# Performance work log

Measured on AMD Instinct MI355X. Metric: run time of the kernel, lower is better.

The kernel has to match this reference:

```python
import jax, jax.numpy as jnp
import numpy as np

N_NODES = 10000
N_EDGES = 100000
F_NODE = 128
F_EDGE = 16
HEADS = 8
OUT_CH = 128  # per-head channels in PyG TransformerConv
HC = HEADS * OUT_CH


def setup_inputs() -> dict:
    key = jax.random.key(0)
    ks = jax.random.split(key, 12)
    sN = 1.0 / np.sqrt(F_NODE)
    sE = 1.0 / np.sqrt(F_EDGE)
    return {
        "x": jax.random.normal(ks[0], (N_NODES, F_NODE), dtype=jnp.float32),
        "edge_attr": jax.random.normal(ks[1], (N_EDGES, F_EDGE), dtype=jnp.float32),
        "edge_index": jax.random.randint(ks[2], (2, N_EDGES), 0, N_NODES, dtype=jnp.int32),
        "Wq": jax.random.normal(ks[3], (F_NODE, HC), dtype=jnp.float32) * sN,
        "bq": jnp.zeros((HC,), dtype=jnp.float32),
        "Wk": jax.random.normal(ks[4], (F_NODE, HC), dtype=jnp.float32) * sN,
        "bk": jnp.zeros((HC,), dtype=jnp.float32),
        "Wv": jax.random.normal(ks[5], (F_NODE, HC), dtype=jnp.float32) * sN,
        "bv": jnp.zeros((HC,), dtype=jnp.float32),
        "We": jax.random.normal(ks[6], (F_EDGE, HC), dtype=jnp.float32) * sE,  # lin_edge has no bias in PyG
        "Wskip": jax.random.normal(ks[7], (F_NODE, OUT_CH), dtype=jnp.float32) * sN,
        "bskip": jnp.zeros((OUT_CH,), dtype=jnp.float32),
        "Wd": jax.random.normal(ks[8], (OUT_CH, 1), dtype=jnp.float32) * (1.0 / np.sqrt(OUT_CH)),
        "bd": jnp.zeros((1,), dtype=jnp.float32),
    }


def reference(x, edge_attr, edge_index, Wq, bq, Wk, bk, Wv, bv, We, Wskip, bskip, Wd, bd):
    N = x.shape[0]
    src, dst = edge_index[0], edge_index[1]  # messages flow src -> dst

    q = (x @ Wq + bq).reshape(N, HEADS, OUT_CH)
    k = (x @ Wk + bk).reshape(N, HEADS, OUT_CH)
    v = (x @ Wv + bv).reshape(N, HEADS, OUT_CH)
    e = (edge_attr @ We).reshape(-1, HEADS, OUT_CH)  # [E, H, C]

    k_j = k[src] + e                        # [E, H, C]
    alpha = jnp.einsum("ehc,ehc->eh", q[dst], k_j) / np.sqrt(OUT_CH)  # [E, H]

    # segment softmax over destination node
    m = jax.ops.segment_max(alpha, dst, num_segments=N)   # [N, H]
    a = jnp.exp(alpha - m[dst])
    s = jax.ops.segment_sum(a, dst, num_segments=N)       # [N, H]
    alpha_n = a / (s[dst] + 1e-16)                        # [E, H]

    msg = (v[src] + e) * alpha_n[:, :, None]              # [E, H, C]
    out = jax.ops.segment_sum(msg, dst, num_segments=N)   # [N, H, C]

    out = out.mean(axis=1)                                # concat=False -> head average, [N, C]
    out = out + x @ Wskip + bskip                         # root/skip connection
    out = jax.nn.relu(out)
    # dropout is identity at inference
    pooled = out.sum(axis=0)                              # [C]
    return pooled @ Wd + bd                               # [1]
```

## Files before the change

### kernel.cpp

```cpp
#include <hip/hip_runtime.h>

#define N_NODES 10000
#define N_EDGES 100000
#define F_NODE 128
#define HEADS 8
#define HC 1024
#define NCOLS2 2432
#define NB2 (NCOLS2 / 128)
#define SLOT_CAP 48

typedef __attribute__((ext_vector_type(8))) short bf16x8;
typedef __attribute__((ext_vector_type(4))) float f32x4;
typedef __attribute__((ext_vector_type(2))) float f32x2;

__device__ __forceinline__ void atomAddF(float* p, float v) {
    unsafeAtomicAdd(p, v);
}
__device__ __forceinline__ unsigned short f2bf(float f) {
    union { float f; unsigned u; } c; c.f = f;
    unsigned u = c.u + 0x7fffu + ((c.u >> 16) & 1u);
    return (unsigned short)(u >> 16);
}
__device__ __forceinline__ float bLo(unsigned x) {
    union { unsigned u; float f; } c; c.u = x << 16; return c.f;
}
__device__ __forceinline__ float bHi(unsigned x) {
    union { unsigned u; float f; } c; c.u = x & 0xffff0000u; return c.f;
}
__device__ __forceinline__ float bf2f(unsigned short u) {
    union { unsigned u; float f; } c; c.u = ((unsigned)u) << 16; return c.f;
}
__device__ __forceinline__ unsigned pk4fp8(unsigned a, unsigned b) {
    int w = __builtin_amdgcn_cvt_pk_fp8_f32(bLo(a), bHi(a), 0, false);
    w = __builtin_amdgcn_cvt_pk_fp8_f32(bLo(b), bHi(b), w, true);
    return (unsigned)w;
}
__device__ __forceinline__ void dq16v(uint4 q, f32x2* f) {
    f[0] = __builtin_amdgcn_cvt_pk_f32_fp8(q.x, false);
    f[1] = __builtin_amdgcn_cvt_pk_f32_fp8(q.x, true);
    f[2] = __builtin_amdgcn_cvt_pk_f32_fp8(q.y, false);
    f[3] = __builtin_amdgcn_cvt_pk_f32_fp8(q.y, true);
    f[4] = __builtin_amdgcn_cvt_pk_f32_fp8(q.z, false);
    f[5] = __builtin_amdgcn_cvt_pk_f32_fp8(q.z, true);
    f[6] = __builtin_amdgcn_cvt_pk_f32_fp8(q.w, false);
    f[7] = __builtin_amdgcn_cvt_pk_f32_fp8(q.w, true);
}
__device__ __forceinline__ void edge_accum2(
    uint4 xq4, uint4 vq4, float2 eav, float svv, bool valid,
    const f32x2* gf2, float qwx, float qwy, float du_r, float scale,
    float& s_reg, float& t0, float& t1, f32x2* va2) {
    f32x2 dac;
    dac.x = eav.x * qwx;
    dac.y = eav.y * qwy;
    f32x2 p;
    p = __builtin_amdgcn_cvt_pk_f32_fp8(xq4.x, false); dac += gf2[0] * p;
    p = __builtin_amdgcn_cvt_pk_f32_fp8(xq4.x, true);  dac += gf2[1] * p;
    p = __builtin_amdgcn_cvt_pk_f32_fp8(xq4.y, false); dac += gf2[2] * p;
    p = __builtin_amdgcn_cvt_pk_f32_fp8(xq4.y, true);  dac += gf2[3] * p;
    p = __builtin_amdgcn_cvt_pk_f32_fp8(xq4.z, false); dac += gf2[4] * p;
    p = __builtin_amdgcn_cvt_pk_f32_fp8(xq4.z, true);  dac += gf2[5] * p;
    p = __builtin_amdgcn_cvt_pk_f32_fp8(xq4.w, false); dac += gf2[6] * p;
    p = __builtin_amdgcn_cvt_pk_f32_fp8(xq4.w, true);  dac += gf2[7] * p;
    float d = dac.x + dac.y;
    d += __shfl_xor(d, 1); d += __shfl_xor(d, 2); d += __shfl_xor(d, 4);
    float a = __expf((d + du_r + svv) * scale);
    a = valid ? a : 0.f;
    s_reg += a;
    t0 += a * eav.x; t1 += a * eav.y;
    f32x2 av; av.x = a; av.y = a;
    p = __builtin_amdgcn_cvt_pk_f32_fp8(vq4.x, false); va2[0] += av * p;
    p = __builtin_amdgcn_cvt_pk_f32_fp8(vq4.x, true);  va2[1] += av * p;
    p = __builtin_amdgcn_cvt_pk_f32_fp8(vq4.y, false); va2[2] += av * p;
    p = __builtin_amdgcn_cvt_pk_f32_fp8(vq4.y, true);  va2[3] += av * p;
    p = __builtin_amdgcn_cvt_pk_f32_fp8(vq4.z, false); va2[4] += av * p;
    p = __builtin_amdgcn_cvt_pk_f32_fp8(vq4.z, true);  va2[5] += av * p;
    p = __builtin_amdgcn_cvt_pk_f32_fp8(vq4.w, false); va2[6] += av * p;
    p = __builtin_amdgcn_cvt_pk_f32_fp8(vq4.w, true);  va2[7] += av * p;
}

#define PREP_A 1250
#define PREP_B (PREP_A + NCOLS2 / 2)
#define PREP_C (PREP_B + 10)
#define PREP_D (PREP_C + 64)
__global__ __launch_bounds__(256) void prep_all(
    const float* __restrict__ x, unsigned short* __restrict__ xb,
    unsigned* __restrict__ xf8, const int* __restrict__ ei,
    int* __restrict__ cnt, int2* __restrict__ slots,
    const float* __restrict__ Wq, const float* __restrict__ Wk,
    const float* __restrict__ Wv, const float* __restrict__ Wskip,
    const float* __restrict__ We, const float* __restrict__ bq,
    const float* __restrict__ bk, const float* __restrict__ bv,
    const float* __restrict__ bskip, unsigned short* __restrict__ wt,
    float* __restrict__ bias, unsigned short* __restrict__ w2t) {
    __shared__ float wesh[2][128];
    __shared__ float wqsh[64][129];
    int tid = threadIdx.x;
    if (blockIdx.x < PREP_A) {
        int i = blockIdx.x * 256 + tid;
        float4 f = ((const float4*)x)[i];
        ushort4 o;
        o.x = f2bf(f.x); o.y = f2bf(f.y); o.z = f2bf(f.z); o.w = f2bf(f.w);
        ((ushort4*)xb)[i] = o;
        int w = __builtin_amdgcn_cvt_pk_fp8_f32(f.x, f.y, 0, false);
        w = __builtin_amdgcn_cvt_pk_fp8_f32(f.z, f.w, w, true);
        xf8[i] = (unsigned)w;
        if (i < N_EDGES) {
            int src = ei[i];
            int dst = ei[N_EDGES + i];
            int pos = atomicAdd(&cnt[dst], 1);
            if (pos < SLOT_CAP) slots[(size_t)dst * SLOT_CAP + pos] = make_int2(src, i);
        }
    } else if (blockIdx.x < PREP_B) {
        int bi = blockIdx.x - PREP_A;
        int cid = tid >> 7, d = tid & 127;
        int n = 2 * bi + cid;
        bool panel = (n < 1024) || (n >= 2176 && n < 2304);
        if (panel) {
            int h = (n < 1024) ? (n >> 7) : ((n - 2176) >> 4);
            if (n < 1024) {
                int f2 = n & 127;
                wesh[cid][d] = Wk[(size_t)f2 * HC + h * 128 + d];
            } else {
                int f = (n - 2176) & 15;
                wesh[cid][d] = We[(size_t)f * HC + h * 128 + d];
            }
            float s = 0.f;
            int c_t = tid & 63, r_t = tid >> 6;
            #pragma unroll 2
            for (int half = 0; half < 2; ++half) {
                #pragma unroll
                for (int rr = 0; rr < 32; ++rr) {
                    int r = rr * 4 + r_t;
                    wqsh[c_t][r] = Wq[(size_t)r * HC + h * 128 + half * 64 + c_t];
                }
                __syncthreads();
                #pragma unroll 16
                for (int cc = 0; cc < 64; ++cc)
                    s += wqsh[cc][d] * wesh[cid][half * 64 + cc];
                __syncthreads();
            }
            wt[(size_t)n * 128 + d] = f2bf(s);
        } else {
            float val;
            if (n < 2048) {
                val = Wv[(size_t)d * HC + (n - 1024)];
            } else if (n < 2176) {
                val = Wskip[(size_t)d * 128 + (n - 2048)];
            } else if (n < 2312) {
                int h = n - 2304;
                wesh[cid][d] = bk[h * 128 + d];
                __syncthreads();
                const float* wq = Wq + (size_t)d * HC + h * 128;
                float s = 0.f;
                #pragma unroll
                for (int c = 0; c < 128; ++c) s += wq[c] * wesh[cid][c];
                val = s;
            } else if (n < 2320) {
                int h = n - 2312;
                wesh[cid][d] = bq[h * 128 + d];
                __syncthreads();
                const float* wk = Wk + (size_t)d * HC + h * 128;
                float s = 0.f;
                #pragma unroll
                for (int c = 0; c < 128; ++c) s += wk[c] * wesh[cid][c];
                val = s;
            } else {
                val = 0.f;
            }
            wt[(size_t)n * 128 + d] = f2bf(val);
        }
    } else if (blockIdx.x < PREP_C) {
        int n = (blockIdx.x - PREP_B) * 256 + tid;
        if (n >= NCOLS2) return;
        float val;
        if (n < 1024) val = 0.f;
        else if (n < 2048) val = bv[n - 1024];
        else if (n < 2176) val = bskip[n - 2048];
        else if (n < 2304) {
            int hf = n - 2176, h = hf >> 4, f = hf & 15;
            float s = 0.f;
            for (int c = 0; c < 128; ++c)
                s += bq[h * 128 + c] * We[(size_t)f * HC + h * 128 + c];
            val = s;
        } else if (n < 2312) {
            int h = n - 2304;
            float s = 0.f;
            for (int c = 0; c < 128; ++c) s += bq[h * 128 + c] * bk[h * 128 + c];
            val = s;
        } else val = 0.f;
        bias[n] = val;
    } else {
        int c = (blockIdx.x - PREP_C) * 2 + (tid >> 7);
        int d = tid & 127;
        int h = d >> 4, f = d & 15;
        w2t[(size_t)c * 128 + d] = f2bf(We[(size_t)f * HC + h * 128 + c] * 0.125f);
    }
}

__global__ __launch_bounds__(256) void gemm_mfma(
    const unsigned short* __restrict__ xb, const unsigned short* __restrict__ wt,
    const float* __restrict__ bias, unsigned char* __restrict__ xgf8,
    unsigned char* __restrict__ vf8, unsigned short* __restrict__ sqb,
    float* __restrict__ du, float* __restrict__ sv) {
    __shared__ unsigned short lds[18432];
    unsigned short (*As)[72] = (unsigned short(*)[72])lds;
    unsigned short (*Bs)[72] = (unsigned short(*)[72])(lds + 9216);
    int tid = threadIdx.x;
    int n0 = blockIdx.x * 128, m0 = blockIdx.y * 128;
    int w = tid >> 6, lane = tid & 63;
    int wm = (w >> 1) * 64, wn = (w & 1) * 64;
    int quad = lane >> 4, l16 = lane & 15;
    f32x4 acc[4][4];
    #pragma unroll
    for (int i = 0; i < 4; ++i)
        #pragma unroll
        for (int j = 0; j < 4; ++j) acc[i][j] = (f32x4){0.f, 0.f, 0.f, 0.f};

    for (int ko = 0; ko < 128; ko += 64) {
        #pragma unroll
        for (int tI = 0; tI < 4; ++tI) {
            int cId = tid + tI * 256;
            int r = cId >> 3, c8 = (cId & 7) << 3;
            int gr = m0 + r;
            uint4 av = make_uint4(0u, 0u, 0u, 0u);
            if (gr < N_NODES)
                av = *(const uint4*)(xb + (size_t)gr * 128 + ko + c8);
            *(uint4*)(&As[r][c8]) = av;
            *(uint4*)(&Bs[r][c8]) =
                *(const uint4*)(wt + (size_t)(n0 + r) * 128 + ko + c8);
        }
        __syncthreads();
        #pragma unroll
        for (int ks = 0; ks < 64; ks += 32) {
            bf16x8 a[4], b[4];
            #pragma unroll
            for (int mt = 0; mt < 4; ++mt)
                a[mt] = *(const bf16x8*)&As[wm + mt * 16 + l16][ks + quad * 8];
            #pragma unroll
            for (int nt = 0; nt < 4; ++nt)
                b[nt] = *(const bf16x8*)&Bs[wn + nt * 16 + l16][ks + quad * 8];
            #pragma unroll
            for (int mt = 0; mt < 4; ++mt)
                #pragma unroll
                for (int nt = 0; nt < 4; ++nt)
                    acc[mt][nt] = __builtin_amdgcn_mfma_f32_16x16x32_bf16(
                        a[mt], b[nt], acc[mt][nt], 0, 0, 0);
        }
        __syncthreads();
    }
    int nt0 = n0 >> 7;
    if (nt0 == 18) {
        #pragma unroll
        for (int mt = 0; mt < 4; ++mt)
            #pragma unroll
            for (int r = 0; r < 4; ++r) {
                int row = m0 + wm + mt * 16 + quad * 4 + r;
                if (row >= N_NODES) continue;
                #pragma unroll
                for (int nt = 0; nt < 4; ++nt) {
                    int col = n0 + wn + nt * 16 + l16;
                    float val = acc[mt][nt][r] + bias[col];
                    if (col < 2312) {
                        du[(size_t)row * 8 + (col - 2304)] = val;
                    } else if (col < 2320) {
                        sv[(size_t)row * 8 + (col - 2312)] = val;
                    }
                }
            }
    } else {
        unsigned short* wst = lds + w * 4608;
        #pragma unroll
        for (int mt = 0; mt < 4; ++mt)
            #pragma unroll
            for (int r = 0; r < 4; ++r) {
                int rl = mt * 16 + quad * 4 + r;
                #pragma unroll
                for (int nt = 0; nt < 4; ++nt) {
                    int cl = nt * 16 + l16;
                    wst[rl * 72 + cl] = f2bf(acc[mt][nt][r] + bias[n0 + wn + cl]);
                }
            }
        __syncthreads();
        if (nt0 < 16) {
            unsigned char* dst = (nt0 < 8) ? xgf8 : vf8;
            int colbase = (n0 & 1023);
            #pragma unroll
            for (int j = 0; j < 4; ++j) {
                int idx = tid + j * 256;
                int r = idx >> 3, c16 = idx & 7;
                int wown = ((r >> 6) << 1) | (c16 >> 2);
                int rl = r & 63;
                const unsigned short* srcp =
                    lds + wown * 4608 + rl * 72 + (c16 & 3) * 16;
                uint4 u0 = *(const uint4*)(srcp);
                uint4 u1 = *(const uint4*)(srcp + 8);
                uint4 o;
                o.x = pk4fp8(u0.x, u0.y);
                o.y = pk4fp8(u0.z, u0.w);
                o.z = pk4fp8(u1.x, u1.y);
                o.w = pk4fp8(u1.z, u1.w);
                int row = m0 + r;
                if (row < N_NODES)
                    *(uint4*)(dst + (size_t)row * 1024 + colbase + c16 * 16) = o;
            }
        } else {
            int colbase = n0 - 2048;
            #pragma unroll
            for (int j = 0; j < 4; ++j) {
                int idx = tid + j * 256;
                int r = idx >> 3, c16 = idx & 7;
                int wown = ((r >> 6) << 1) | (c16 >> 2);
                int rl = r & 63;
                const unsigned short* srcp =
                    lds + wown * 4608 + rl * 72 + (c16 & 3) * 16;
                uint4 u0 = *(const uint4*)(srcp);
                uint4 u1 = *(const uint4*)(srcp + 8);
                int row = m0 + r;
                if (row < N_NODES) {
                    uint4* dp = (uint4*)(sqb + (size_t)row * 256 + colbase + c16 * 16);
                    dp[0] = u0;
                    dp[1] = u1;
                }
            }
        }
    }
}

__global__ __launch_bounds__(256) void node_kernel(
    const unsigned char* __restrict__ xgf8, const unsigned char* __restrict__ xf8,
    const unsigned char* __restrict__ vf8, const unsigned short* __restrict__ sqb,
    const float* __restrict__ ea, const float* __restrict__ du,
    const float* __restrict__ sv, const int2* __restrict__ slots,
    const int* __restrict__ cnt, unsigned short* __restrict__ ttb,
    float* __restrict__ hsum) {
    int t = threadIdx.x;
    int w = t >> 6, lane = t & 63;
    int lh = lane & 7, h = lane >> 3;
    const float scale = 0.08838834764831845f;
    int n = __builtin_amdgcn_readfirstlane(blockIdx.x * 4 + w);

    uint4 gq = *(const uint4*)(xgf8 + (size_t)n * 1024 + 16 * lane);
    f32x2 gf2[8];
    dq16v(gq, gf2);
    ushort2 qwu = *(const ushort2*)(sqb + (size_t)n * 256 + 128 + h * 16 + 2 * lh);
    float qwx = bf2f(qwu.x), qwy = bf2f(qwu.y);
    float du_r = du[(size_t)n * 8 + h];

    int cn = cnt[n];
    cn = (cn > SLOT_CAP) ? SLOT_CAP : cn;
    cn = __builtin_amdgcn_readfirstlane(cn);
    const int2* sp = slots + (size_t)n * SLOT_CAP;
    const unsigned char* eab = (const unsigned char*)ea;

    unsigned xoff = lh * 16u;
    unsigned voff = lane * 16u;
    unsigned eoff = lh * 8u;

    f32x2 va2[8];
    #pragma unroll
    for (int i = 0; i < 8; ++i) va2[i] = (f32x2){0.f, 0.f};
    float s_reg = 0.f, t0 = 0.f, t1 = 0.f;

    if (cn > 0) {
        int np = (cn + 1) >> 1;
        uint4 x0A = {}, x0B = {}, v0A = {}, v0B = {};
        uint4 x1A = {}, x1B = {}, v1A = {}, v1B = {};
        float2 e0A = {}, e0B = {}, e1A = {}, e1B = {};
        float sv0A = 0.f, sv0B = 0.f, sv1A = 0.f, sv1B = 0.f;
        bool m0B = false, m1B = false;

#define LOADP(xA, xB, vA, vB, eA, eB, svA, svB, mB, pp) do {                    \
        int _p = (pp);                                                          \
        if (_p < np) {                                                          \
            int _i0 = 2 * _p;                                                   \
            bool _mb = (_i0 + 1) < cn;                                          \
            int2 _sa = sp[_i0];                                                 \
            int2 _sb = sp[_mb ? _i0 + 1 : _i0];                                 \
            mB = _mb;                                                           \
            xA = *(const uint4*)(xf8 + (((unsigned)_sa.x) << 7) + xoff);        \
            xB = *(const uint4*)(xf8 + (((unsigned)_sb.x) << 7) + xoff);        \
            vA = *(const uint4*)(vf8 + (((unsigned)_sa.x) << 10) + voff);       \
            vB = *(const uint4*)(vf8 + (((unsigned)_sb.x) << 10) + voff);       \
            eA = *(const float2*)(eab + (((unsigned)_sa.y) << 6) + eoff);       \
            eB = *(const float2*)(eab + (((unsigned)_sb.y) << 6) + eoff);       \
            svA = sv[(((unsigned)_sa.x) << 3) + h];                             \
            svB = sv[(((unsigned)_sb.x) << 3) + h];                             \
        }                                                                       \
    } while (0)

        LOADP(x0A, x0B, v0A, v0B, e0A, e0B, sv0A, sv0B, m0B, 0);
        LOADP(x1A, x1B, v1A, v1B, e1A, e1B, sv1A, sv1B, m1B, 1);
        int p = 0;
        while (true) {
            if (p >= np) break;
            edge_accum2(x0A, v0A, e0A, sv0A, true, gf2, qwx, qwy, du_r, scale,
                        s_reg, t0, t1, va2);
            edge_accum2(x0B, v0B, e0B, sv0B, m0B, gf2, qwx, qwy, du_r, scale,
                        s_reg, t0, t1, va2);
            LOADP(x0A, x0B, v0A, v0B, e0A, e0B, sv0A, sv0B, m0B, p + 2);
            ++p;
            if (p >= np) break;
            edge_accum2(x1A, v1A, e1A, sv1A, true, gf2, qwx, qwy, du_r, scale,
                        s_reg, t0, t1, va2);
            edge_accum2(x1B, v1B, e1B, sv1B, m1B, gf2, qwx, qwy, du_r, scale,
                        s_reg, t0, t1, va2);
            LOADP(x1A, x1B, v1A, v1B, e1A, e1B, sv1A, sv1B, m1B, p + 2);
            ++p;
        }
#undef LOADP
    }

    float inv = 1.f / (s_reg + 1e-16f);
    ushort2 tw;
    tw.x = f2bf(t0 * inv);
    tw.y = f2bf(t1 * inv);
    *(ushort2*)(ttb + (size_t)n * 128 + h * 16 + 2 * lh) = tw;
    float sc = inv * 0.125f;
    float va[16];
    #pragma unroll
    for (int i = 0; i < 8; ++i) { va[2 * i] = va2[i].x; va[2 * i + 1] = va2[i].y; }
    #pragma unroll
    for (int i = 0; i < 16; ++i) {
        float o = va[i] * sc;
        o += __shfl_xor(o, 8);
        o += __shfl_xor(o, 16);
        o += __shfl_xor(o, 32);
        va[i] = o;
    }
    if (lane < 8) {
        float* hp = hsum + (size_t)n * 128 + lane * 16;
        #pragma unroll
        for (int p2 = 0; p2 < 4; ++p2) {
            float4 h4 = make_float4(va[4 * p2], va[4 * p2 + 1],
                                    va[4 * p2 + 2], va[4 * p2 + 3]);
            ((float4*)hp)[p2] = h4;
        }
    }
}

__global__ __launch_bounds__(256) void out_gemm(
    const unsigned short* __restrict__ ttb, const unsigned short* __restrict__ w2t,
    const float* __restrict__ hsum, const unsigned short* __restrict__ sqb,
    float* __restrict__ pooled, int* __restrict__ done,
    const float* __restrict__ Wd, const float* __restrict__ bd,
    float* __restrict__ out) {
    __shared__ unsigned short As[64][136];
    __shared__ float pool_sh[128];
    __shared__ int last_sh;
    int tid = threadIdx.x;
    int m0 = blockIdx.x * 64;
    int w = tid >> 6, lane = tid & 63;
    int wm = (w >> 1) * 32, wn = (w & 1) * 64;
    int quad = lane >> 4, l16 = lane & 15;
    if (tid < 128) pool_sh[tid] = 0.f;
    #pragma unroll
    for (int tI = 0; tI < 4; ++tI) {
        int cId = tid + tI * 256;
        int r = cId >> 4, c8 = (cId & 15) << 3;
        int gr = m0 + r;
        uint4 av = make_uint4(0u, 0u, 0u, 0u);
        if (gr < N_NODES)
            av = *(const uint4*)(ttb + (size_t)gr * 128 + c8);
        *(uint4*)(&As[r][c8]) = av;
    }
    __syncthreads();
    f32x4 acc[2][4];
    #pragma unroll
    for (int i = 0; i < 2; ++i)
        #pragma unroll
        for (int j = 0; j < 4; ++j) acc[i][j] = (f32x4){0.f, 0.f, 0.f, 0.f};

    const unsigned short* bb = w2t + (size_t)(wn + l16) * 128 + quad * 8;
    #pragma unroll
    for (int ks = 0; ks < 128; ks += 32) {
        bf16x8 a[2], b[4];
        #pragma unroll
        for (int mt = 0; mt < 2; ++mt)
            a[mt] = *(const bf16x8*)&As[wm + mt * 16 + l16][ks + quad * 8];
        #pragma unroll
        for (int nt = 0; nt < 4; ++nt)
            b[nt] = *(const bf16x8*)(bb + (size_t)nt * 16 * 128 + ks);
        #pragma unroll
        for (int mt = 0; mt < 2; ++mt)
            #pragma unroll
            for (int nt = 0; nt < 4; ++nt)
                acc[mt][nt] = __builtin_amdgcn_mfma_f32_16x16x32_bf16(
                    a[mt], b[nt], acc[mt][nt], 0, 0, 0);
    }
    float pl[4] = {0.f, 0.f, 0.f, 0.f};
    #pragma unroll
    for (int mt = 0; mt < 2; ++mt) {
        #pragma unroll
        for (int r = 0; r < 4; ++r) {
            int row = m0 + wm + mt * 16 + quad * 4 + r;
            if (row >= N_NODES) continue;
            #pragma unroll
            for (int nt = 0; nt < 4; ++nt) {
                int col = wn + nt * 16 + l16;
                float val = acc[mt][nt][r] + hsum[(size_t)row * 128 + col]
                            + bf2f(sqb[(size_t)row * 256 + col]);
                pl[nt] += fmaxf(val, 0.f);
            }
        }
    }
    #pragma unroll
    for (int nt = 0; nt < 4; ++nt)
        atomicAdd(&pool_sh[wn + nt * 16 + l16], pl[nt]);
    __syncthreads();
    if (tid < 128) atomAddF(&pooled[tid], pool_sh[tid]);
    __threadfence();
    if (tid == 0) last_sh = (atomicAdd(done, 1) == (int)gridDim.x - 1);
    __syncthreads();
    if (last_sh && tid < 64) {
        float p0 = __hip_atomic_load(&pooled[2 * tid], __ATOMIC_RELAXED,
                                     __HIP_MEMORY_SCOPE_AGENT);
        float p1 = __hip_atomic_load(&pooled[2 * tid + 1], __ATOMIC_RELAXED,
                                     __HIP_MEMORY_SCOPE_AGENT);
        float vv = p0 * Wd[2 * tid] + p1 * Wd[2 * tid + 1];
        vv += __shfl_xor(vv, 1);  vv += __shfl_xor(vv, 2);  vv += __shfl_xor(vv, 4);
        vv += __shfl_xor(vv, 8);  vv += __shfl_xor(vv, 16); vv += __shfl_xor(vv, 32);
        if (tid == 0) out[0] = vv + bd[0];
    }
}

extern "C" void kernel_launch(void* const* d_in, const int* in_sizes, int n_in,
                              void* d_out, int out_size, void* d_ws, size_t ws_size,
                              hipStream_t stream) {
    const float* x     = (const float*)d_in[0];
    const float* eattr = (const float*)d_in[1];
    const int*   ei    = (const int*)d_in[2];
    const float* Wq    = (const float*)d_in[3];
    const float* bq    = (const float*)d_in[4];
    const float* Wk    = (const float*)d_in[5];
    const float* bk    = (const float*)d_in[6];
    const float* Wv    = (const float*)d_in[7];
    const float* bv    = (const float*)d_in[8];
    const float* We    = (const float*)d_in[9];
    const float* Wskip = (const float*)d_in[10];
    const float* bskip = (const float*)d_in[11];
    const float* Wd    = (const float*)d_in[12];
    const float* bd    = (const float*)d_in[13];
    float* out = (float*)d_out;

    char* ws = (char*)d_ws;
    unsigned char*  xgf8 = (unsigned char*)(ws + 0);
    unsigned char*  vf8  = (unsigned char*)(ws + 10240000);
    unsigned short* sqb  = (unsigned short*)(ws + 20480000);
    float* hsum = (float*)(ws + 25600000);
    unsigned short* xb   = (unsigned short*)(ws + 30720000);
    unsigned short* ttb  = xb;
    unsigned*       xf8  = (unsigned*)(ws + 33280000);
    float* du   = (float*)(ws + 34560000);
    float* sv   = (float*)(ws + 34880000);
    unsigned short* wt   = (unsigned short*)(ws + 35200000);
    float* bias = (float*)(ws + 35822592);
    unsigned short* w2t  = (unsigned short*)(ws + 35832320);
    int* cnt    = (int*)(ws + 35865088);
    float* pooled = (float*)(ws + 35905088);
    int* done   = (int*)(ws + 35905600);
    int2* slots = (int2*)(ws + 35905616);

    hipMemsetAsync(cnt, 0, 40000 + 512 + 16, stream);

    prep_all<<<PREP_D, 256, 0, stream>>>(
        x, xb, xf8, ei, cnt, slots, Wq, Wk, Wv, Wskip, We, bq, bk, bv, bskip,
        wt, bias, w2t);

    gemm_mfma<<<dim3(NB2, (N_NODES + 127) / 128), 256, 0, stream>>>(
        xb, wt, bias, xgf8, vf8, sqb, du, sv);

    node_kernel<<<N_NODES / 4, 256, 0, stream>>>(
        xgf8, (const unsigned char*)xf8, vf8, sqb, eattr, du, sv, slots, cnt,
        ttb, hsum);

    out_gemm<<<(N_NODES + 63) / 64, 256, 0, stream>>>(
        ttb, w2t, hsum, sqb, pooled, done, Wd, bd, out);
}
```

Measured before the change: 169.6 us.

## Compute folded Wq·Wk and Wq·We weight panels with bf16 MFMA blocks

The prep kernel's per-head Wq^T·Wk and Wq^T·We weight folding used to be scalar FP32 dot products, one output column per thread-half and many blocks. Each head's panel is now computed by a single block: the tiles are staged as bf16 in LDS and multiplied with 16x16x32 bf16 MFMA. The remaining column-copy and bias work is remapped into a separate block range. This cuts redundant Wq loads and scalar FLOPs in preprocessing, but the folded weights now come from bf16-rounded inputs, which lowers their precision. Only 8 blocks per panel type run, so parallelism in this phase drops.

New measurement: 169.1 us. About the same (-0.3%).

```diff
diff --git a/kernel.cpp b/kernel.cpp
--- a/kernel.cpp
+++ b/kernel.cpp
@@ -79,8 +79,10 @@
 }
 
 #define PREP_A 1250
-#define PREP_B (PREP_A + NCOLS2 / 2)
-#define PREP_C (PREP_B + 10)
+#define PREP_G (PREP_A + 8)
+#define PREP_Q (PREP_G + 8)
+#define PREP_R (PREP_Q + 640)
+#define PREP_C (PREP_R + 10)
 #define PREP_D (PREP_C + 64)
 __global__ __launch_bounds__(256) void prep_all(
     const float* __restrict__ x, unsigned short* __restrict__ xb,
@@ -93,7 +95,8 @@
     const float* __restrict__ bskip, unsigned short* __restrict__ wt,
     float* __restrict__ bias, unsigned short* __restrict__ w2t) {
     __shared__ float wesh[2][128];
-    __shared__ float wqsh[64][129];
+    __shared__ unsigned short wlA[128][136];
+    __shared__ unsigned short wlB[128][136];
     int tid = threadIdx.x;
     if (blockIdx.x < PREP_A) {
         int i = blockIdx.x * 256 + tid;
@@ -110,67 +113,133 @@
             int pos = atomicAdd(&cnt[dst], 1);
             if (pos < SLOT_CAP) slots[(size_t)dst * SLOT_CAP + pos] = make_int2(src, i);
         }
-    } else if (blockIdx.x < PREP_B) {
-        int bi = blockIdx.x - PREP_A;
+    } else if (blockIdx.x < PREP_G) {
+        int h = blockIdx.x - PREP_A;
+        #pragma unroll
+        for (int pass = 0; pass < 16; ++pass) {
+            int idx = pass * 256 + tid;
+            int r = idx >> 5, c4 = (idx & 31) << 2;
+            float4 a = *(const float4*)(Wk + (size_t)r * HC + h * 128 + c4);
+            float4 b = *(const float4*)(Wq + (size_t)r * HC + h * 128 + c4);
+            ushort4 ua, ub;
+            ua.x = f2bf(a.x); ua.y = f2bf(a.y); ua.z = f2bf(a.z); ua.w = f2bf(a.w);
+            ub.x = f2bf(b.x); ub.y = f2bf(b.y); ub.z = f2bf(b.z); ub.w = f2bf(b.w);
+            *(ushort4*)(&wlA[r][c4]) = ua;
+            *(ushort4*)(&wlB[r][c4]) = ub;
+        }
+        __syncthreads();
+        int w = tid >> 6, lane = tid & 63;
+        int wm = (w >> 1) * 64, wn = (w & 1) * 64;
+        int quad = lane >> 4, l16 = lane & 15;
+        f32x4 acc[4][4];
+        #pragma unroll
+        for (int i = 0; i < 4; ++i)
+            #pragma unroll
+            for (int j = 0; j < 4; ++j) acc[i][j] = (f32x4){0.f, 0.f, 0.f, 0.f};
+        #pragma unroll
+        for (int ks = 0; ks < 128; ks += 32) {
+            bf16x8 a[4], b[4];
+            #pragma unroll
+            for (int mt = 0; mt < 4; ++mt)
+                a[mt] = *(const bf16x8*)&wlA[wm + mt * 16 + l16][ks + quad * 8];
+            #pragma unroll
+            for (int nt = 0; nt < 4; ++nt)
+                b[nt] = *(const bf16x8*)&wlB[wn + nt * 16 + l16][ks + quad * 8];
+            #pragma unroll
+            for (int mt = 0; mt < 4; ++mt)
+                #pragma unroll
+                for (int nt = 0; nt < 4; ++nt)
+                    acc[mt][nt] = __builtin_amdgcn_mfma_f32_16x16x32_bf16(
+                        a[mt], b[nt], acc[mt][nt], 0, 0, 0);
+        }
+        #pragma unroll
+        for (int mt = 0; mt < 4; ++mt)
+            #pragma unroll
+            for (int r2 = 0; r2 < 4; ++r2) {
+                int f2 = wm + mt * 16 + quad * 4 + r2;
+                #pragma unroll
+                for (int nt = 0; nt < 4; ++nt) {
+                    int d = wn + nt * 16 + l16;
+                    wt[(size_t)(h * 128 + f2) * 128 + d] = f2bf(acc[mt][nt][r2]);
+                }
+            }
+    } else if (blockIdx.x < PREP_Q) {
+        int h = blockIdx.x - PREP_G;
+        #pragma unroll
+        for (int pass = 0; pass < 16; ++pass) {
+            int idx = pass * 256 + tid;
+            int r = idx >> 5, c4 = (idx & 31) << 2;
+            float4 b = *(const float4*)(Wq + (size_t)r * HC + h * 128 + c4);
+            ushort4 ub;
+            ub.x = f2bf(b.x); ub.y = f2bf(b.y); ub.z = f2bf(b.z); ub.w = f2bf(b.w);
+            *(ushort4*)(&wlB[r][c4]) = ub;
+        }
+        #pragma unroll
+        for (int pass = 0; pass < 2; ++pass) {
+            int idx = pass * 256 + tid;
+            int r = idx >> 5, c4 = (idx & 31) << 2;
+            float4 a = *(const float4*)(We + (size_t)r * HC + h * 128 + c4);
+            ushort4 ua;
+            ua.x = f2bf(a.x); ua.y = f2bf(a.y); ua.z = f2bf(a.z); ua.w = f2bf(a.w);
+            *(ushort4*)(&wlA[r][c4]) = ua;
+        }
+        __syncthreads();
+        int w = tid >> 6, lane = tid & 63;
+        int quad = lane >> 4, l16 = lane & 15;
+        int wn = w * 32;
+        f32x4 acc[2];
+        acc[0] = (f32x4){0.f, 0.f, 0.f, 0.f};
+        acc[1] = (f32x4){0.f, 0.f, 0.f, 0.f};
+        #pragma unroll
+        for (int ks = 0; ks < 128; ks += 32) {
+            bf16x8 a = *(const bf16x8*)&wlA[l16][ks + quad * 8];
+            #pragma unroll
+            for (int nt = 0; nt < 2; ++nt) {
+                bf16x8 b = *(const bf16x8*)&wlB[wn + nt * 16 + l16][ks + quad * 8];
+                acc[nt] = __builtin_amdgcn_mfma_f32_16x16x32_bf16(a, b, acc[nt], 0, 0, 0);
+            }
+        }
+        #pragma unroll
+        for (int nt = 0; nt < 2; ++nt)
+            #pragma unroll
+            for (int r2 = 0; r2 < 4; ++r2) {
+                int f = quad * 4 + r2;
+                int d = wn + nt * 16 + l16;
+                wt[(size_t)(2176 + h * 16 + f) * 128 + d] = f2bf(acc[nt][r2]);
+            }
+    } else if (blockIdx.x < PREP_R) {
+        int j = blockIdx.x - PREP_Q;
         int cid = tid >> 7, d = tid & 127;
-        int n = 2 * bi + cid;
-        bool panel = (n < 1024) || (n >= 2176 && n < 2304);
-        if (panel) {
-            int h = (n < 1024) ? (n >> 7) : ((n - 2176) >> 4);
-            if (n < 1024) {
-                int f2 = n & 127;
-                wesh[cid][d] = Wk[(size_t)f2 * HC + h * 128 + d];
-            } else {
-                int f = (n - 2176) & 15;
-                wesh[cid][d] = We[(size_t)f * HC + h * 128 + d];
-            }
+        int n = (j < 576) ? (1024 + 2 * j + cid) : (2304 + 2 * (j - 576) + cid);
+        float val;
+        if (n < 2048) {
+            val = Wv[(size_t)d * HC + (n - 1024)];
+        } else if (n < 2176) {
+            val = Wskip[(size_t)d * 128 + (n - 2048)];
+        } else if (n < 2312) {
+            int h = n - 2304;
+            wesh[cid][d] = bk[h * 128 + d];
+            __syncthreads();
+            const float* wq = Wq + (size_t)d * HC + h * 128;
             float s = 0.f;
-            int c_t = tid & 63, r_t = tid >> 6;
-            #pragma unroll 2
-            for (int half = 0; half < 2; ++half) {
-                #pragma unroll
-                for (int rr = 0; rr < 32; ++rr) {
-                    int r = rr * 4 + r_t;
-                    wqsh[c_t][r] = Wq[(size_t)r * HC + h * 128 + half * 64 + c_t];
-                }
-                __syncthreads();
-                #pragma unroll 16
-                for (int cc = 0; cc < 64; ++cc)
-                    s += wqsh[cc][d] * wesh[cid][half * 64 + cc];
-                __syncthreads();
-            }
-            wt[(size_t)n * 128 + d] = f2bf(s);
+            #pragma unroll
+            for (int c = 0; c < 128; ++c) s += wq[c] * wesh[cid][c];
+            val = s;
+        } else if (n < 2320) {
+            int h = n - 2312;
+            wesh[cid][d] = bq[h * 128 + d];
+            __syncthreads();
+            const float* wk = Wk + (size_t)d * HC + h * 128;
+            float s = 0.f;
+            #pragma unroll
+            for (int c = 0; c < 128; ++c) s += wk[c] * wesh[cid][c];
+            val = s;
         } else {
-            float val;
-            if (n < 2048) {
-                val = Wv[(size_t)d * HC + (n - 1024)];
-            } else if (n < 2176) {
-                val = Wskip[(size_t)d * 128 + (n - 2048)];
-            } else if (n < 2312) {
-                int h = n - 2304;
-                wesh[cid][d] = bk[h * 128 + d];
-                __syncthreads();
-                const float* wq = Wq + (size_t)d * HC + h * 128;
-                float s = 0.f;
-                #pragma unroll
-                for (int c = 0; c < 128; ++c) s += wq[c] * wesh[cid][c];
-                val = s;
-            } else if (n < 2320) {
-                int h = n - 2312;
-                wesh[cid][d] = bq[h * 128 + d];
-                __syncthreads();
-                const float* wk = Wk + (size_t)d * HC + h * 128;
-                float s = 0.f;
-                #pragma unroll
-                for (int c = 0; c < 128; ++c) s += wk[c] * wesh[cid][c];
-                val = s;
-            } else {
-                val = 0.f;
-            }
-            wt[(size_t)n * 128 + d] = f2bf(val);
-        }
+            val = 0.f;
+        }
+        wt[(size_t)n * 128 + d] = f2bf(val);
     } else if (blockIdx.x < PREP_C) {
-        int n = (blockIdx.x - PREP_B) * 256 + tid;
+        int n = (blockIdx.x - PREP_R) * 256 + tid;
         if (n >= NCOLS2) return;
         float val;
         if (n < 1024) val = 0.f;
```
